# Optimization experiments

Hardware: AMD Instinct MI355X
Metric: run time of the kernel (lower is better)

The kernel has to match this reference:

```python
import jax, jax.numpy as jnp
import numpy as np

GAMMA = 0.1   # permanent impact coef
ETA = 0.3     # temporary impact coef
B = 2_000_000
FEATURE_DIM = 32
HIDDEN = 64


def setup_inputs() -> dict:
    key = jax.random.key(0)
    k_os, k_liq, k_w1, k_b1, k_w2, k_b2 = jax.random.split(key, 6)
    order_sizes = jax.random.normal(k_os, (B,), dtype=jnp.float32) * 500.0
    # liquidity must be positive (used under sqrt and as divisor); scale ~ market_depth=1000
    liquidity = jax.random.uniform(k_liq, (B,), dtype=jnp.float32) * 1000.0 + 100.0
    # encoder params: Linear(3,64) -> ReLU -> Linear(64,32) -> LayerNorm(32)
    lim1 = 1.0 / np.sqrt(3.0)
    lim2 = 1.0 / np.sqrt(HIDDEN)
    W1 = jax.random.uniform(k_w1, (3, HIDDEN), dtype=jnp.float32, minval=-lim1, maxval=lim1)
    b1 = jax.random.uniform(k_b1, (HIDDEN,), dtype=jnp.float32, minval=-lim1, maxval=lim1)
    W2 = jax.random.uniform(k_w2, (HIDDEN, FEATURE_DIM), dtype=jnp.float32, minval=-lim2, maxval=lim2)
    b2 = jax.random.uniform(k_b2, (FEATURE_DIM,), dtype=jnp.float32, minval=-lim2, maxval=lim2)
    ln_w = jnp.ones((FEATURE_DIM,), dtype=jnp.float32)
    ln_b = jnp.zeros((FEATURE_DIM,), dtype=jnp.float32)
    return {"order_sizes": order_sizes, "liquidity": liquidity,
            "W1": W1, "b1": b1, "W2": W2, "b2": b2, "ln_w": ln_w, "ln_b": ln_b}


def _layernorm(x, w, b, eps=1e-5):
    mu = jnp.mean(x, axis=-1, keepdims=True)
    var = jnp.var(x, axis=-1, keepdims=True)
    return (x - mu) * jax.lax.rsqrt(var + eps) * w + b


def reference(order_sizes, liquidity, W1, b1, W2, b2, ln_w, ln_b):
    # vectorized replacement of the per-element .item() loop
    perm = GAMMA * order_sizes / liquidity                                   # [B]
    temp = ETA * jnp.sign(order_sizes) * jnp.sqrt(jnp.abs(order_sizes)) / jnp.sqrt(liquidity)  # [B]
    total = perm + temp                                                      # [B]
    feats = jnp.stack([perm, temp, total], axis=1)                           # [B, 3]
    h = jax.nn.relu(feats @ W1 + b1)                                         # [B, 64]
    encoded = _layernorm(h @ W2 + b2, ln_w, ln_b)                            # [B, 32]
    return perm, temp, total, encoded
```

## Files before the change

### kernel.cpp

```cpp
#include <hip/hip_runtime.h>

#define GAMMA 0.1f
#define ETA   0.3f

typedef __attribute__((ext_vector_type(8))) short short8;
typedef __attribute__((ext_vector_type(4))) float f32x4;

#define ITERS 2

__device__ __forceinline__ short f2bf(float x) {
    unsigned u = __float_as_uint(x);
    u += 0x7FFFu + ((u >> 16) & 1u);
    return (short)(u >> 16);
}

__global__ __launch_bounds__(256) void market_impact_mfma(
    const float* __restrict__ os_g, const float* __restrict__ liq_g,
    const float* __restrict__ W1,  const float* __restrict__ b1g,
    const float* __restrict__ W2,  const float* __restrict__ b2,
    const float* __restrict__ lnw, const float* __restrict__ lnb,
    float* __restrict__ out, int B)
{
    const int tid  = threadIdx.x;
    const int lane = tid & 63;
    const int g    = lane >> 4;
    const int c    = lane & 15;

    float u[16], v[16], bb[16];
    #pragma unroll
    for (int kc = 0; kc < 2; ++kc)
        #pragma unroll
        for (int j = 0; j < 8; ++j) {
            int k = kc * 32 + g * 8 + j;
            float w0 = W1[k], w1 = W1[64 + k], w2r = W1[128 + k];
            u[kc * 8 + j]  = w0 + w2r;
            v[kc * 8 + j]  = w1 + w2r;
            bb[kc * 8 + j] = b1g[k];
        }

    short8 wfrag[2][2];
    #pragma unroll
    for (int kc = 0; kc < 2; ++kc)
        #pragma unroll
        for (int cc = 0; cc < 2; ++cc) {
            short8 t;
            #pragma unroll
            for (int j = 0; j < 8; ++j) {
                int k = kc * 32 + g * 8 + j;
                t[j] = f2bf(W2[k * 32 + cc * 16 + c]);
            }
            wfrag[kc][cc] = t;
        }

    float b2a[8], lnwa[8], lnba[8];
    #pragma unroll
    for (int cc = 0; cc < 2; ++cc) {
        float4 bq = *reinterpret_cast<const float4*>(b2  + cc * 16 + g * 4);
        float4 wq = *reinterpret_cast<const float4*>(lnw + cc * 16 + g * 4);
        float4 bl = *reinterpret_cast<const float4*>(lnb + cc * 16 + g * 4);
        b2a[cc*4+0] = bq.x; b2a[cc*4+1] = bq.y; b2a[cc*4+2] = bq.z; b2a[cc*4+3] = bq.w;
        lnwa[cc*4+0] = wq.x; lnwa[cc*4+1] = wq.y; lnwa[cc*4+2] = wq.z; lnwa[cc*4+3] = wq.w;
        lnba[cc*4+0] = bl.x; lnba[cc*4+1] = bl.y; lnba[cc*4+2] = bl.z; lnba[cc*4+3] = bl.w;
    }

    const long long wid = (long long)blockIdx.x * 4 + (tid >> 6);
    float* enc = out + 3LL * B;

    #pragma unroll 1
    for (int it = 0; it < ITERS; ++it) {
        long long base = (wid * ITERS + it) * 64;
        if (base >= B) break;

        int r  = (int)base + lane;
        bool ok = r < B;
        float o  = ok ? os_g[r]  : 0.f;
        float lq = ok ? liq_g[r] : 1.f;
        float perm = GAMMA * o / lq;
        float temp = ETA * copysignf(sqrtf(fabsf(o)), o) * rsqrtf(lq);
        float tot  = perm + temp;
        if (ok) {
            out[r]         = perm;
            out[B + r]     = temp;
            out[2 * B + r] = tot;
        }

        #pragma unroll
        for (int mt = 0; mt < 4; ++mt) {
            float pm = __shfl(perm, mt * 16 + c);
            float tm = __shfl(temp, mt * 16 + c);
            short8 a0, a1;
            #pragma unroll
            for (int j = 0; j < 8; ++j) {
                float h0 = fmaxf(0.f, fmaf(pm, u[j],     fmaf(tm, v[j],     bb[j])));
                float h1 = fmaxf(0.f, fmaf(pm, u[8 + j], fmaf(tm, v[8 + j], bb[8 + j])));
                a0[j] = f2bf(h0);
                a1[j] = f2bf(h1);
            }

            f32x4 d0 = {0.f, 0.f, 0.f, 0.f};
            f32x4 d1 = {0.f, 0.f, 0.f, 0.f};
            d0 = __builtin_amdgcn_mfma_f32_16x16x32_bf16(wfrag[0][0], a0, d0, 0, 0, 0);
            d0 = __builtin_amdgcn_mfma_f32_16x16x32_bf16(wfrag[1][0], a1, d0, 0, 0, 0);
            d1 = __builtin_amdgcn_mfma_f32_16x16x32_bf16(wfrag[0][1], a0, d1, 0, 0, 0);
            d1 = __builtin_amdgcn_mfma_f32_16x16x32_bf16(wfrag[1][1], a1, d1, 0, 0, 0);

            float x[8];
            #pragma unroll
            for (int reg = 0; reg < 4; ++reg) {
                x[reg]     = d0[reg] + b2a[reg];
                x[4 + reg] = d1[reg] + b2a[4 + reg];
            }
            float s = 0.f, q = 0.f;
            #pragma unroll
            for (int j = 0; j < 8; ++j) { s += x[j]; q = fmaf(x[j], x[j], q); }
            s += __shfl_xor(s, 16); s += __shfl_xor(s, 32);
            q += __shfl_xor(q, 16); q += __shfl_xor(q, 32);
            float mu   = s * 0.03125f;
            float var  = fmaf(q, 0.03125f, -mu * mu);
            float rstd = rsqrtf(var + 1e-5f);

            int row = (int)base + mt * 16 + c;
            if (row < B) {
                float4 o0, o1;
                o0.x = fmaf((x[0] - mu) * rstd, lnwa[0], lnba[0]);
                o0.y = fmaf((x[1] - mu) * rstd, lnwa[1], lnba[1]);
                o0.z = fmaf((x[2] - mu) * rstd, lnwa[2], lnba[2]);
                o0.w = fmaf((x[3] - mu) * rstd, lnwa[3], lnba[3]);
                o1.x = fmaf((x[4] - mu) * rstd, lnwa[4], lnba[4]);
                o1.y = fmaf((x[5] - mu) * rstd, lnwa[5], lnba[5]);
                o1.z = fmaf((x[6] - mu) * rstd, lnwa[6], lnba[6]);
                o1.w = fmaf((x[7] - mu) * rstd, lnwa[7], lnba[7]);
                float* rp = enc + (long long)row * 32;
                *reinterpret_cast<float4*>(rp + g * 4)      = o0;
                *reinterpret_cast<float4*>(rp + 16 + g * 4) = o1;
            }
        }
    }
}

extern "C" void kernel_launch(void* const* d_in, const int* in_sizes, int n_in,
                              void* d_out, int out_size, void* d_ws, size_t ws_size,
                              hipStream_t stream) {
    const float* os_g = (const float*)d_in[0];
    const float* liq  = (const float*)d_in[1];
    const float* W1   = (const float*)d_in[2];
    const float* b1   = (const float*)d_in[3];
    const float* W2   = (const float*)d_in[4];
    const float* b2   = (const float*)d_in[5];
    const float* lnw  = (const float*)d_in[6];
    const float* lnb  = (const float*)d_in[7];
    float* out = (float*)d_out;
    const int B = in_sizes[0];

    const int rows_per_block = 4 * ITERS * 64;
    const int grid = (B + rows_per_block - 1) / rows_per_block;
    market_impact_mfma<<<grid, 256, 0, stream>>>(
        os_g, liq, W1, b1, W2, b2, lnw, lnb, out, B);
}
```

Baseline: 86.08 us.

## Prefetch next chunk inputs, fold bias into MFMA accumulator, use fast intrinsics

Each wave now handles four 64-row chunks instead of two, with a launch-bounds occupancy hint. The next chunk's order_sizes and liquidity are prefetched into registers while the current chunk computes, to hide load latency. The b2 bias is preloaded into the MFMA accumulator, which removes separate adds. The IEEE divide, sqrt and rsqrt are replaced with the AMD hardware rcp/sqrt/rsq intrinsics, trading some accuracy for fewer instructions.

```diff
diff --git a/kernel.cpp b/kernel.cpp
--- a/kernel.cpp
+++ b/kernel.cpp
@@ -2,11 +2,10 @@
 
 #define GAMMA 0.1f
 #define ETA   0.3f
+#define ITERS 4
 
 typedef __attribute__((ext_vector_type(8))) short short8;
 typedef __attribute__((ext_vector_type(4))) float f32x4;
-
-#define ITERS 2
 
 __device__ __forceinline__ short f2bf(float x) {
     unsigned u = __float_as_uint(x);
@@ -14,7 +13,7 @@
     return (short)(u >> 16);
 }
 
-__global__ __launch_bounds__(256) void market_impact_mfma(
+__global__ __launch_bounds__(256, 4) void market_impact_mfma(
     const float* __restrict__ os_g, const float* __restrict__ liq_g,
     const float* __restrict__ W1,  const float* __restrict__ b1g,
     const float* __restrict__ W2,  const float* __restrict__ b2,
@@ -63,25 +62,38 @@
         lnba[cc*4+0] = bl.x; lnba[cc*4+1] = bl.y; lnba[cc*4+2] = bl.z; lnba[cc*4+3] = bl.w;
     }
 
-    const long long wid = (long long)blockIdx.x * 4 + (tid >> 6);
+    const int wid = blockIdx.x * 4 + (tid >> 6);
+    const long long base = (long long)wid * (ITERS * 64);
     float* enc = out + 3LL * B;
+
+    int   pr  = (int)base + lane;
+    bool  pok = (base + lane) < (long long)B;
+    float o_n = pok ? os_g[pr]  : 0.f;
+    float l_n = pok ? liq_g[pr] : 1.f;
 
     #pragma unroll 1
     for (int it = 0; it < ITERS; ++it) {
-        long long base = (wid * ITERS + it) * 64;
-        if (base >= B) break;
+        long long cbase = base + it * 64;
+        if (cbase >= B) break;
 
-        int r  = (int)base + lane;
+        float o = o_n, lq = l_n;
+        int   r = (int)cbase + lane;
         bool ok = r < B;
-        float o  = ok ? os_g[r]  : 0.f;
-        float lq = ok ? liq_g[r] : 1.f;
-        float perm = GAMMA * o / lq;
-        float temp = ETA * copysignf(sqrtf(fabsf(o)), o) * rsqrtf(lq);
-        float tot  = perm + temp;
+
+        if (it + 1 < ITERS) {
+            int nr = r + 64;
+            bool nok = nr < B;
+            o_n = nok ? os_g[nr]  : 0.f;
+            l_n = nok ? liq_g[nr] : 1.f;
+        }
+
+        float perm = GAMMA * o * __builtin_amdgcn_rcpf(lq);
+        float temp = ETA * copysignf(__builtin_amdgcn_sqrtf(fabsf(o)), o)
+                         * __builtin_amdgcn_rsqf(lq);
         if (ok) {
             out[r]         = perm;
             out[B + r]     = temp;
-            out[2 * B + r] = tot;
+            out[2 * B + r] = perm + temp;
         }
 
         #pragma unroll
@@ -97,39 +109,36 @@
                 a1[j] = f2bf(h1);
             }
 
-            f32x4 d0 = {0.f, 0.f, 0.f, 0.f};
-            f32x4 d1 = {0.f, 0.f, 0.f, 0.f};
+            f32x4 d0 = {b2a[0], b2a[1], b2a[2], b2a[3]};
+            f32x4 d1 = {b2a[4], b2a[5], b2a[6], b2a[7]};
             d0 = __builtin_amdgcn_mfma_f32_16x16x32_bf16(wfrag[0][0], a0, d0, 0, 0, 0);
             d0 = __builtin_amdgcn_mfma_f32_16x16x32_bf16(wfrag[1][0], a1, d0, 0, 0, 0);
             d1 = __builtin_amdgcn_mfma_f32_16x16x32_bf16(wfrag[0][1], a0, d1, 0, 0, 0);
             d1 = __builtin_amdgcn_mfma_f32_16x16x32_bf16(wfrag[1][1], a1, d1, 0, 0, 0);
 
-            float x[8];
+            float s = 0.f, q = 0.f;
             #pragma unroll
             for (int reg = 0; reg < 4; ++reg) {
-                x[reg]     = d0[reg] + b2a[reg];
-                x[4 + reg] = d1[reg] + b2a[4 + reg];
+                s += d0[reg];  q = fmaf(d0[reg], d0[reg], q);
+                s += d1[reg];  q = fmaf(d1[reg], d1[reg], q);
             }
-            float s = 0.f, q = 0.f;
-            #pragma unroll
-            for (int j = 0; j < 8; ++j) { s += x[j]; q = fmaf(x[j], x[j], q); }
             s += __shfl_xor(s, 16); s += __shfl_xor(s, 32);
             q += __shfl_xor(q, 16); q += __shfl_xor(q, 32);
             float mu   = s * 0.03125f;
             float var  = fmaf(q, 0.03125f, -mu * mu);
-            float rstd = rsqrtf(var + 1e-5f);
+            float rstd = __builtin_amdgcn_rsqf(var + 1e-5f);
 
-            int row = (int)base + mt * 16 + c;
+            int row = (int)cbase + mt * 16 + c;
             if (row < B) {
                 float4 o0, o1;
-                o0.x = fmaf((x[0] - mu) * rstd, lnwa[0], lnba[0]);
-                o0.y = fmaf((x[1] - mu) * rstd, lnwa[1], lnba[1]);
-                o0.z = fmaf((x[2] - mu) * rstd, lnwa[2], lnba[2]);
-                o0.w = fmaf((x[3] - mu) * rstd, lnwa[3], lnba[3]);
-                o1.x = fmaf((x[4] - mu) * rstd, lnwa[4], lnba[4]);
-                o1.y = fmaf((x[5] - mu) * rstd, lnwa[5], lnba[5]);
-                o1.z = fmaf((x[6] - mu) * rstd, lnwa[6], lnba[6]);
-                o1.w = fmaf((x[7] - mu) * rstd, lnwa[7], lnba[7]);
+                o0.x = fmaf((d0[0] - mu) * rstd, lnwa[0], lnba[0]);
+                o0.y = fmaf((d0[1] - mu) * rstd, lnwa[1], lnba[1]);
+                o0.z = fmaf((d0[2] - mu) * rstd, lnwa[2], lnba[2]);
+                o0.w = fmaf((d0[3] - mu) * rstd, lnwa[3], lnba[3]);
+                o1.x = fmaf((d1[0] - mu) * rstd, lnwa[4], lnba[4]);
+                o1.y = fmaf((d1[1] - mu) * rstd, lnwa[5], lnba[5]);
+                o1.z = fmaf((d1[2] - mu) * rstd, lnwa[6], lnba[6]);
+                o1.w = fmaf((d1[3] - mu) * rstd, lnwa[7], lnba[7]);
                 float* rp = enc + (long long)row * 32;
                 *reinterpret_cast<float4*>(rp + g * 4)      = o0;
                 *reinterpret_cast<float4*>(rp + 16 + g * 4) = o1;
```

After: 117.6 us. +36.7%, slower.
